# Performance work log

Measured on AMD Instinct MI355X. Metric: run time of the kernel, lower is better.

The kernel has to match this reference:

```python
import jax, jax.numpy as jnp
import numpy as np

CL = 64      # per-object feature dim
N = 8        # num objects/slots
B = 8192     # batch


def _init(key, fan_in, shape):
    # torch Linear default: U(-1/sqrt(fan_in), 1/sqrt(fan_in))
    bound = 1.0 / np.sqrt(fan_in)
    return jax.random.uniform(key, shape, jnp.float32, -bound, bound)


def setup_inputs() -> dict:
    key = jax.random.key(0)
    ks = jax.random.split(key, 20)
    inp = {
        "s": jax.random.normal(ks[0], (B, N, CL), jnp.float32),
        # weights stored (in, out); y = x @ W + b
        "W_enc": _init(ks[1], CL, (CL, CL)),   "b_enc": _init(ks[2], CL, (CL,)),
        "W_self0": _init(ks[3], CL, (CL, CL)), "b_self0": _init(ks[4], CL, (CL,)),
        "W_self1": _init(ks[5], CL, (CL, CL)), "b_self1": _init(ks[6], CL, (CL,)),
        "W_rel0": _init(ks[7], 2 * CL + 1, (2 * CL + 1, 2 * CL)), "b_rel0": _init(ks[8], 2 * CL + 1, (2 * CL,)),
        "W_rel1": _init(ks[9], 2 * CL, (2 * CL, CL)),             "b_rel1": _init(ks[10], 2 * CL, (CL,)),
        "W_rel2": _init(ks[11], CL, (CL, CL)),                    "b_rel2": _init(ks[12], CL, (CL,)),
        "W_att0": _init(ks[13], 2 * CL + 1, (2 * CL + 1, 2 * CL)), "b_att0": _init(ks[14], 2 * CL + 1, (2 * CL,)),
        "W_att1": _init(ks[15], 2 * CL, (2 * CL, CL)),             "b_att1": _init(ks[16], 2 * CL, (CL,)),
        "W_att2": _init(ks[17], CL, (CL, 1)),                      "b_att2": _init(ks[18], CL, (1,)),
    }
    return inp


def reference(s, W_enc, b_enc, W_self0, b_self0, W_self1, b_self1,
              W_rel0, b_rel0, W_rel1, b_rel1, W_rel2, b_rel2,
              W_att0, b_att0, W_att1, b_att1, W_att2, b_att2):
    elu = jax.nn.elu
    # keep first 2 coords (positions), re-encode the rest
    s = jnp.concatenate([s[..., :2], (s @ W_enc + b_enc)[..., 2:]], axis=-1)  # [B,N,CL]

    # self dynamics
    h = elu(s @ W_self0 + b_self0)
    self_dyn = h @ W_self1 + b_self1 + h                                      # [B,N,CL]

    # pairwise squared distances on first two coords: [B,N,N,1]
    pos = s[..., :2]
    dist = jnp.sum((pos[:, :, None, :] - pos[:, None, :, :]) ** 2, axis=-1, keepdims=True)

    # combinations = cat(arg1_i, arg2_j, dist). Split the first linear's weight rows
    # so we never materialize the [B,N,N,2CL+1] concat tensor.
    def pair_linear(W, b):
        Wa, Wb, Wd = W[:CL], W[CL:2 * CL], W[2 * CL]
        return (s @ Wa)[:, :, None, :] + (s @ Wb)[:, None, :, :] + dist * Wd + b

    rel_h1 = elu(pair_linear(W_rel0, b_rel0))        # [B,N,N,2CL]
    rel_h2 = elu(rel_h1 @ W_rel1 + b_rel1)           # [B,N,N,CL]
    rel_f = rel_h2 @ W_rel2 + b_rel2 + rel_h2        # [B,N,N,CL]

    att = elu(pair_linear(W_att0, b_att0))
    att = elu(att @ W_att1 + b_att1)
    att = jax.nn.sigmoid(att @ W_att2 + b_att2)      # [B,N,N,1]

    diag_mask = (1.0 - jnp.eye(N, dtype=s.dtype))[None, :, :, None]
    rel_dyn = jnp.sum(rel_f * diag_mask * att, axis=2)   # [B,N,CL]

    return jnp.sum(self_dyn + rel_dyn, axis=1)           # [B,CL]
```

## Files before the change

### kernel.cpp

```cpp
#include <hip/hip_runtime.h>
#include <math.h>

constexpr int NCL = 64;
constexpr int NN  = 8;
constexpr int NG  = 4;
constexpr int NT  = 1024;

typedef __attribute__((ext_vector_type(4))) float f32x4;
typedef __attribute__((ext_vector_type(8))) short s16x8;
#define MFMA __builtin_amdgcn_mfma_f32_16x16x32_bf16

constexpr int OFF_ENC = 0;
constexpr int OFF_S0  = 1024;
constexpr int OFF_S1  = 2048;
constexpr int OFF_R0  = 3072;
constexpr int OFF_A0  = 7168;
constexpr int OFF_A1  = 11264;
constexpr int OFF_R1  = 13312;
constexpr int OFF_R2  = 15360;

__device__ __forceinline__ float elu_f(float x) { return x > 0.f ? x : __expf(x) - 1.f; }

__device__ __forceinline__ unsigned f2u(float x) { union { float f; unsigned u; } c; c.f = x; return c.u; }
__device__ __forceinline__ float u2f(unsigned u) { union { unsigned u; float f; } c; c.u = u; return c.f; }

__device__ __forceinline__ void splitpack8(const float v[8], s16x8& hi, s16x8& lo) {
    union { s16x8 s; unsigned u[4]; } H, L;
    #pragma unroll
    for (int e = 0; e < 8; e += 2) {
        H.u[e >> 1] = __builtin_amdgcn_perm(f2u(v[e + 1]), f2u(v[e]), 0x07060302u);
        const float t0 = u2f(f2u(v[e])     & 0xffff0000u);
        const float t1 = u2f(f2u(v[e + 1]) & 0xffff0000u);
        L.u[e >> 1] = __builtin_amdgcn_perm(f2u(v[e + 1] - t1), f2u(v[e] - t0), 0x07060302u);
    }
    hi = H.s; lo = L.s;
}

__device__ __forceinline__ void afrag_split(const float* act, int row, int kbase,
                                            s16x8& hi, s16x8& lo) {
    const float4 v0 = *(const float4*)(act + row * 68 + kbase);
    const float4 v1 = *(const float4*)(act + row * 68 + kbase + 4);
    const float v[8] = {v0.x, v0.y, v0.z, v0.w, v1.x, v1.y, v1.z, v1.w};
    splitpack8(v, hi, lo);
}

__device__ __forceinline__ f32x4 node_tile_pk(const float* act, const s16x8* __restrict__ wb,
                                              int mt, int nt, int lane) {
    const int row = mt * 16 + (lane & 15);
    const int g   = lane >> 4;
    f32x4 acc = {0.f, 0.f, 0.f, 0.f};
    #pragma unroll
    for (int kg = 0; kg < 2; ++kg) {
        s16x8 ah, al;
        afrag_split(act, row, kg * 32 + g * 8, ah, al);
        const s16x8 bh = wb[(kg * 4 + nt) * 64 + lane];
        const s16x8 bl = wb[512 + (kg * 4 + nt) * 64 + lane];
        acc = MFMA(ah, bh, acc, 0, 0, 0);
        acc = MFMA(ah, bl, acc, 0, 0, 0);
        acc = MFMA(al, bh, acc, 0, 0, 0);
    }
    return acc;
}

__device__ __forceinline__ void x1frag(const float* Arow, const float* Brow,
                                       const float* wdg, float d, int fbase,
                                       s16x8& hi, s16x8& lo) {
    const float4 a0 = *(const float4*)(Arow + fbase);
    const float4 a1 = *(const float4*)(Arow + fbase + 4);
    const float4 c0 = *(const float4*)(Brow + fbase);
    const float4 c1 = *(const float4*)(Brow + fbase + 4);
    const float4 w0 = *(const float4*)(wdg + fbase);
    const float4 w1 = *(const float4*)(wdg + fbase + 4);
    float v[8];
    v[0] = elu_f(fmaf(d, w0.x, a0.x + c0.x));
    v[1] = elu_f(fmaf(d, w0.y, a0.y + c0.y));
    v[2] = elu_f(fmaf(d, w0.z, a0.z + c0.z));
    v[3] = elu_f(fmaf(d, w0.w, a0.w + c0.w));
    v[4] = elu_f(fmaf(d, w1.x, a1.x + c1.x));
    v[5] = elu_f(fmaf(d, w1.y, a1.y + c1.y));
    v[6] = elu_f(fmaf(d, w1.z, a1.z + c1.z));
    v[7] = elu_f(fmaf(d, w1.w, a1.w + c1.w));
    splitpack8(v, hi, lo);
}

__device__ __forceinline__ short bfh_rn(float x) {
    union { float f; unsigned u; } c; c.f = x;
    return (short)((c.u + 0x7fffu + ((c.u >> 16) & 1u)) >> 16);
}
__device__ __forceinline__ void split_tr(float x, short& hi, short& lo) {
    union { float f; unsigned u; } c; c.f = x;
    hi = (short)(c.u >> 16);
    union { unsigned u; float f; } t; t.u = c.u & 0xffff0000u;
    lo = bfh_rn(x - t.f);
}

__global__ __launch_bounds__(64)
void prep_kernel(const float* __restrict__ We,  const float* __restrict__ Ws0,
                 const float* __restrict__ Ws1, const float* __restrict__ Wr0,
                 const float* __restrict__ Wa0, const float* __restrict__ Wa1,
                 const float* __restrict__ Wr1, const float* __restrict__ Wr2,
                 s16x8* __restrict__ ws)
{
    const int b = blockIdx.x, lane = threadIdx.x;
    const float* W; int nnt, nfrag, base, frag;
    if      (b < 8)   { W = We;  nnt = 4; nfrag = 8;  base = OFF_ENC; frag = b; }
    else if (b < 16)  { W = Ws0; nnt = 4; nfrag = 8;  base = OFF_S0;  frag = b - 8; }
    else if (b < 24)  { W = Ws1; nnt = 4; nfrag = 8;  base = OFF_S1;  frag = b - 16; }
    else if (b < 56)  { W = Wr0; nnt = 8; nfrag = 32; base = OFF_R0;  frag = b - 24; }
    else if (b < 88)  { W = Wa0; nnt = 8; nfrag = 32; base = OFF_A0;  frag = b - 56; }
    else if (b < 104) { W = Wa1; nnt = 4; nfrag = 16; base = OFF_A1;  frag = b - 88; }
    else if (b < 120) { W = Wr1; nnt = 4; nfrag = 16; base = OFF_R1;  frag = b - 104; }
    else              { W = Wr2; nnt = 4; nfrag = 8;  base = OFF_R2;  frag = b - 120; }
    const int kg = frag / nnt, nt = frag % nnt;
    const int N  = nnt * 16;
    const int g  = lane >> 4, col = nt * 16 + (lane & 15);
    s16x8 hi, lo;
    #pragma unroll
    for (int e = 0; e < 8; ++e) {
        short a, c; split_tr(W[(kg * 32 + g * 8 + e) * N + col], a, c);
        hi[e] = a; lo[e] = c;
    }
    ws[base + frag * 64 + lane]              = hi;
    ws[base + nfrag * 64 + frag * 64 + lane] = lo;
}

__global__ __launch_bounds__(NT, 1)
void gh_kernel(const float* __restrict__ S,
               const float* __restrict__ b_enc,
               const float* __restrict__ b_self0, const float* __restrict__ b_self1,
               const float* __restrict__ W_rel0,  const float* __restrict__ b_rel0,
               const float* __restrict__ b_rel1,  const float* __restrict__ b_rel2,
               const float* __restrict__ W_att0,  const float* __restrict__ b_att0,
               const float* __restrict__ b_att1,
               const float* __restrict__ W_att2,  const float* __restrict__ b_att2,
               const s16x8* __restrict__ wp,
               float* __restrict__ Out)
{
    __shared__ __align__(16) float sbuf[32 * 68];
    __shared__ __align__(16) float encb[32 * 68];
    __shared__ __align__(16) float hbuf[32 * 68];
    __shared__ __align__(16) float ABm[4][32 * 132];
    __shared__ __align__(16) s16x8 wstpA[2048];
    __shared__ __align__(16) s16x8 wstpR[2048];
    __shared__ float d2l[4 * 64];
    __shared__ float cntl[32];
    __shared__ float wdl[2][128];

    const int tid  = threadIdx.x;
    const int w    = tid >> 6;
    const int lane = tid & 63;
    const int g    = lane >> 4;
    const int b0   = blockIdx.x * NG;
    float* sd   = sbuf;
    float* Tb   = hbuf;
    float* Ubuf = encb;
    float* Rbuf = encb + 512;

    {
        const float* src = S + (size_t)b0 * NN * NCL;
        for (int idx = tid; idx < 32 * 64; idx += NT)
            sbuf[(idx >> 6) * 68 + (idx & 63)] = src[idx];
        for (int idx = tid; idx < 2048; idx += NT) {
            wstpA[idx] = wp[OFF_A1 + idx];
            wstpR[idx] = wp[OFF_R1 + idx];
        }
        if (tid < 128) {
            wdl[0][tid] = W_rel0[128 * 128 + tid];
            wdl[1][tid] = W_att0[128 * 128 + tid];
        }
    }
    __syncthreads();

    if (tid < 256) {
        const int bi = tid >> 6, i = (tid >> 3) & 7, j = tid & 7;
        const float dx = sbuf[(bi * 8 + i) * 68 + 0] - sbuf[(bi * 8 + j) * 68 + 0];
        const float dy = sbuf[(bi * 8 + i) * 68 + 1] - sbuf[(bi * 8 + j) * 68 + 1];
        d2l[bi * 64 + i * 8 + j] = dx * dx + dy * dy;
    }

    if (w < 8) {
        const int mt = w & 1, nt = w >> 1;
        f32x4 acc = node_tile_pk(sbuf, wp + OFF_ENC, mt, nt, lane);
        const int   col = nt * 16 + (lane & 15);
        const float be  = b_enc[col];
        #pragma unroll
        for (int reg = 0; reg < 4; ++reg) {
            const int row = mt * 16 + g * 4 + reg;
            float v = acc[reg] + be;
            if (col < 2) v = sbuf[row * 68 + col];
            encb[row * 68 + col] = v;
        }
    }
    __syncthreads();

    if (w < 8) {
        const int mt = w & 1, nt = w >> 1;
        f32x4 acc = node_tile_pk(encb, wp + OFF_S0, mt, nt, lane);
        const int   col = nt * 16 + (lane & 15);
        const float bs  = b_self0[col];
        #pragma unroll
        for (int reg = 0; reg < 4; ++reg)
            hbuf[(mt * 16 + g * 4 + reg) * 68 + col] = elu_f(acc[reg] + bs);
    }
    __syncthreads();

    if (w < 8) {
        const int mt = w & 1, nt = w >> 1;
        f32x4 acc = node_tile_pk(hbuf, wp + OFF_S1, mt, nt, lane);
        const int   col = nt * 16 + (lane & 15);
        const float bs  = b_self1[col];
        #pragma unroll
        for (int reg = 0; reg < 4; ++reg) {
            const int row = mt * 16 + g * 4 + reg;
            sd[row * 68 + col] = acc[reg] + bs + hbuf[row * 68 + col];
        }
    }
    {
        const int mtp = w >> 3, ntp = w & 7;
        const int row = mtp * 16 + (lane & 15);
        const int col = ntp * 16 + (lane & 15);
        s16x8 eh[2], el[2];
        afrag_split(encb, row, g * 8, eh[0], el[0]);
        afrag_split(encb, row, 32 + g * 8, eh[1], el[1]);
        #pragma unroll
        for (int m = 0; m < 4; ++m) {
            const s16x8* wb = wp + ((m < 2) ? OFF_R0 : OFF_A0);
            const int kgo = (m & 1) * 2;
            f32x4 acc = {0.f, 0.f, 0.f, 0.f};
            #pragma unroll
            for (int kg = 0; kg < 2; ++kg) {
                const s16x8 bh = wb[((kgo + kg) * 8 + ntp) * 64 + lane];
                const s16x8 bl = wb[2048 + ((kgo + kg) * 8 + ntp) * 64 + lane];
                acc = MFMA(eh[kg], bh, acc, 0, 0, 0);
                acc = MFMA(eh[kg], bl, acc, 0, 0, 0);
                acc = MFMA(el[kg], bh, acc, 0, 0, 0);
            }
            const float badd = (m == 0) ? b_rel0[col] : (m == 2) ? b_att0[col] : 0.f;
            #pragma unroll
            for (int reg = 0; reg < 4; ++reg)
                ABm[m][(mtp * 16 + g * 4 + reg) * 132 + col] = acc[reg] + badd;
        }
    }
    __syncthreads();

    const int bi    = w >> 2;
    const int ihalf = (w >> 1) & 1;
    const int mt    = w & 1;
    const int pp    = (lane & 15) + 16 * mt;
    const int il    = pp >> 3, jj8 = pp & 7;
    const float* Arow_a = &ABm[2][(bi * 8 + ihalf * 4 + il) * 132];
    const float* Brow_a = &ABm[3][(bi * 8 + jj8) * 132];
    const float* Arow_r = &ABm[0][(bi * 8 + ihalf * 4 + il) * 132];
    const float* Brow_r = &ABm[1][(bi * 8 + jj8) * 132];
    const float dpair   = d2l[bi * 64 + (ihalf * 4 + il) * 8 + jj8];

    float attreg[4];
    {
        const float ba2 = b_att2[0];
        float wa2v[4];
        f32x4 acc[4];
        #pragma unroll
        for (int nt = 0; nt < 4; ++nt) {
            wa2v[nt] = W_att2[nt * 16 + (lane & 15)];
            const float b1 = b_att1[nt * 16 + (lane & 15)];
            acc[nt] = {b1, b1, b1, b1};
        }
        #pragma unroll
        for (int kg = 0; kg < 4; ++kg) {
            s16x8 ah, al;
            x1frag(Arow_a, Brow_a, &wdl[1][0], dpair, kg * 32 + g * 8, ah, al);
            #pragma unroll
            for (int nt = 0; nt < 4; ++nt) {
                const s16x8 bh = wstpA[(kg * 4 + nt) * 64 + lane];
                const s16x8 bl = wstpA[1024 + (kg * 4 + nt) * 64 + lane];
                acc[nt] = MFMA(ah, bh, acc[nt], 0, 0, 0);
                acc[nt] = MFMA(ah, bl, acc[nt], 0, 0, 0);
                acc[nt] = MFMA(al, bh, acc[nt], 0, 0, 0);
            }
        }
        #pragma unroll
        for (int reg = 0; reg < 4; ++reg) {
            float s = 0.f;
            #pragma unroll
            for (int nt = 0; nt < 4; ++nt) s += elu_f(acc[nt][reg]) * wa2v[nt];
            s += __shfl_xor(s, 1, 64);
            s += __shfl_xor(s, 2, 64);
            s += __shfl_xor(s, 4, 64);
            s += __shfl_xor(s, 8, 64);
            attreg[reg] = 1.f / (1.f + __expf(-(s + ba2)));
        }
    }
    {
        f32x4 acc[4];
        #pragma unroll
        for (int nt = 0; nt < 4; ++nt) {
            const float b1 = b_rel1[nt * 16 + (lane & 15)];
            acc[nt] = {b1, b1, b1, b1};
        }
        #pragma unroll
        for (int kg = 0; kg < 4; ++kg) {
            s16x8 ah, al;
            x1frag(Arow_r, Brow_r, &wdl[0][0], dpair, kg * 32 + g * 8, ah, al);
            #pragma unroll
            for (int nt = 0; nt < 4; ++nt) {
                const s16x8 bh = wstpR[(kg * 4 + nt) * 64 + lane];
                const s16x8 bl = wstpR[1024 + (kg * 4 + nt) * 64 + lane];
                acc[nt] = MFMA(ah, bh, acc[nt], 0, 0, 0);
                acc[nt] = MFMA(ah, bl, acc[nt], 0, 0, 0);
                acc[nt] = MFMA(al, bh, acc[nt], 0, 0, 0);
            }
        }
        const int ifull = ihalf * 4 + 2 * mt + (g >> 1);
        float coef[4], cpart = 0.f;
        #pragma unroll
        for (int reg = 0; reg < 4; ++reg) {
            const int jj = 4 * (g & 1) + reg;
            coef[reg] = (jj == ifull) ? 0.f : attreg[reg];
            cpart += coef[reg];
        }
        const float csum = cpart + __shfl_xor(cpart, 16, 64);
        if (((g & 1) == 0) && ((lane & 15) == 0))
            cntl[bi * 8 + ifull] = csum;
        #pragma unroll
        for (int nt = 0; nt < 4; ++nt) {
            float tpart = 0.f;
            #pragma unroll
            for (int reg = 0; reg < 4; ++reg)
                tpart += coef[reg] * elu_f(acc[nt][reg]);
            const float tsum = tpart + __shfl_xor(tpart, 16, 64);
            if ((g & 1) == 0)
                Tb[(bi * 8 + ifull) * 68 + nt * 16 + (lane & 15)] = tsum;
        }
    }
    __syncthreads();

    if (tid < 256) {
        const int b = tid >> 6, c = tid & 63;
        float u = 0.f;
        #pragma unroll
        for (int i = 0; i < 8; ++i) u += Tb[(b * 8 + i) * 68 + c];
        Ubuf[b * 68 + c] = u;
    }
    __syncthreads();

    if (w < 4) {
        const int nt2 = w;
        f32x4 acc = {0.f, 0.f, 0.f, 0.f};
        const int row = lane & 15;
        #pragma unroll
        for (int kg = 0; kg < 2; ++kg) {
            float4 q0 = {0.f, 0.f, 0.f, 0.f}, q1 = {0.f, 0.f, 0.f, 0.f};
            if (row < 4) {
                q0 = *(const float4*)(Ubuf + row * 68 + kg * 32 + g * 8);
                q1 = *(const float4*)(Ubuf + row * 68 + kg * 32 + g * 8 + 4);
            }
            const float v[8] = {q0.x, q0.y, q0.z, q0.w, q1.x, q1.y, q1.z, q1.w};
            s16x8 uh, ul;
            splitpack8(v, uh, ul);
            const s16x8 bh = wp[OFF_R2 + (kg * 4 + nt2) * 64 + lane];
            const s16x8 bl = wp[OFF_R2 + 512 + (kg * 4 + nt2) * 64 + lane];
            acc = MFMA(uh, bh, acc, 0, 0, 0);
            acc = MFMA(uh, bl, acc, 0, 0, 0);
            acc = MFMA(ul, bh, acc, 0, 0, 0);
        }
        if (g == 0) {
            #pragma unroll
            for (int reg = 0; reg < 4; ++reg)
                Rbuf[reg * 64 + nt2 * 16 + (lane & 15)] = acc[reg];
        }
    }
    __syncthreads();

    if (tid < 256) {
        const int b = tid >> 6, c = tid & 63;
        float sds = 0.f, C = 0.f;
        #pragma unroll
        for (int i = 0; i < 8; ++i) {
            sds += sd[(b * 8 + i) * 68 + c];
            C   += cntl[b * 8 + i];
        }
        Out[(size_t)(b0 + b) * 64 + c] = sds + Rbuf[b * 64 + c] + C * b_rel2[c] + Ubuf[b * 68 + c];
    }
}

extern "C" void kernel_launch(void* const* d_in, const int* in_sizes, int n_in,
                              void* d_out, int out_size, void* d_ws, size_t ws_size,
                              hipStream_t stream) {
    const float* S       = (const float*)d_in[0];
    const float* W_enc   = (const float*)d_in[1];
    const float* b_enc   = (const float*)d_in[2];
    const float* W_self0 = (const float*)d_in[3];
    const float* b_self0 = (const float*)d_in[4];
    const float* W_self1 = (const float*)d_in[5];
    const float* b_self1 = (const float*)d_in[6];
    const float* W_rel0  = (const float*)d_in[7];
    const float* b_rel0  = (const float*)d_in[8];
    const float* W_rel1  = (const float*)d_in[9];
    const float* b_rel1  = (const float*)d_in[10];
    const float* W_rel2  = (const float*)d_in[11];
    const float* b_rel2  = (const float*)d_in[12];
    const float* W_att0  = (const float*)d_in[13];
    const float* b_att0  = (const float*)d_in[14];
    const float* W_att1  = (const float*)d_in[15];
    const float* b_att1  = (const float*)d_in[16];
    const float* W_att2  = (const float*)d_in[17];
    const float* b_att2  = (const float*)d_in[18];

    s16x8* wpk = (s16x8*)d_ws;

    prep_kernel<<<dim3(128), dim3(64), 0, stream>>>(
        W_enc, W_self0, W_self1, W_rel0, W_att0, W_att1, W_rel1, W_rel2, wpk);

    const int nB   = in_sizes[0] / (NN * NCL);
    const int grid = nB / NG;

    gh_kernel<<<dim3(grid), dim3(NT), 0, stream>>>(
        S, b_enc, b_self0, b_self1,
        W_rel0, b_rel0, b_rel1, b_rel2,
        W_att0, b_att0, b_att1, W_att2, b_att2,
        wpk, (float*)d_out);
}
```

Measured before the change: 223.6 us.

## Halve block size to two batches per block and read pair weights from global

Shrinks each block from 4 batch elements with 1024 threads to 2 batch elements with 512 threads. It also drops the LDS staging of the att1/rel1 weight fragments, which now come straight from global memory (through L1/L2). Together these cut LDS use per block so several blocks can share a CU, with launch bounds raised to allow that. The cost is repeated global loads of the weight fragments in the inner MFMA loop and some per-block setup overhead repeated across twice as many blocks.

```diff
diff --git a/kernel.cpp b/kernel.cpp
--- a/kernel.cpp
+++ b/kernel.cpp
@@ -3,8 +3,8 @@
 
 constexpr int NCL = 64;
 constexpr int NN  = 8;
-constexpr int NG  = 4;
-constexpr int NT  = 1024;
+constexpr int NG  = 2;
+constexpr int NT  = 512;
 
 typedef __attribute__((ext_vector_type(4))) float f32x4;
 typedef __attribute__((ext_vector_type(8))) short s16x8;
@@ -124,7 +124,7 @@
     ws[base + nfrag * 64 + frag * 64 + lane] = lo;
 }
 
-__global__ __launch_bounds__(NT, 1)
+__global__ __launch_bounds__(NT, 6)
 void gh_kernel(const float* __restrict__ S,
                const float* __restrict__ b_enc,
                const float* __restrict__ b_self0, const float* __restrict__ b_self1,
@@ -136,14 +136,12 @@
                const s16x8* __restrict__ wp,
                float* __restrict__ Out)
 {
-    __shared__ __align__(16) float sbuf[32 * 68];
-    __shared__ __align__(16) float encb[32 * 68];
-    __shared__ __align__(16) float hbuf[32 * 68];
-    __shared__ __align__(16) float ABm[4][32 * 132];
-    __shared__ __align__(16) s16x8 wstpA[2048];
-    __shared__ __align__(16) s16x8 wstpR[2048];
-    __shared__ float d2l[4 * 64];
-    __shared__ float cntl[32];
+    __shared__ __align__(16) float sbuf[16 * 68];
+    __shared__ __align__(16) float encb[16 * 68];
+    __shared__ __align__(16) float hbuf[16 * 68];
+    __shared__ __align__(16) float ABm[4][16 * 132];
+    __shared__ float d2l[2 * 64];
+    __shared__ float cntl[16];
     __shared__ float wdl[2][128];
 
     const int tid  = threadIdx.x;
@@ -158,12 +156,8 @@
 
     {
         const float* src = S + (size_t)b0 * NN * NCL;
-        for (int idx = tid; idx < 32 * 64; idx += NT)
+        for (int idx = tid; idx < 16 * 64; idx += NT)
             sbuf[(idx >> 6) * 68 + (idx & 63)] = src[idx];
-        for (int idx = tid; idx < 2048; idx += NT) {
-            wstpA[idx] = wp[OFF_A1 + idx];
-            wstpR[idx] = wp[OFF_R1 + idx];
-        }
         if (tid < 128) {
             wdl[0][tid] = W_rel0[128 * 128 + tid];
             wdl[1][tid] = W_att0[128 * 128 + tid];
@@ -171,21 +165,21 @@
     }
     __syncthreads();
 
-    if (tid < 256) {
+    if (tid < 128) {
         const int bi = tid >> 6, i = (tid >> 3) & 7, j = tid & 7;
         const float dx = sbuf[(bi * 8 + i) * 68 + 0] - sbuf[(bi * 8 + j) * 68 + 0];
         const float dy = sbuf[(bi * 8 + i) * 68 + 1] - sbuf[(bi * 8 + j) * 68 + 1];
         d2l[bi * 64 + i * 8 + j] = dx * dx + dy * dy;
     }
 
-    if (w < 8) {
-        const int mt = w & 1, nt = w >> 1;
-        f32x4 acc = node_tile_pk(sbuf, wp + OFF_ENC, mt, nt, lane);
+    if (w < 4) {
+        const int nt = w;
+        f32x4 acc = node_tile_pk(sbuf, wp + OFF_ENC, 0, nt, lane);
         const int   col = nt * 16 + (lane & 15);
         const float be  = b_enc[col];
         #pragma unroll
         for (int reg = 0; reg < 4; ++reg) {
-            const int row = mt * 16 + g * 4 + reg;
+            const int row = g * 4 + reg;
             float v = acc[reg] + be;
             if (col < 2) v = sbuf[row * 68 + col];
             encb[row * 68 + col] = v;
@@ -193,31 +187,31 @@
     }
     __syncthreads();
 
-    if (w < 8) {
-        const int mt = w & 1, nt = w >> 1;
-        f32x4 acc = node_tile_pk(encb, wp + OFF_S0, mt, nt, lane);
+    if (w < 4) {
+        const int nt = w;
+        f32x4 acc = node_tile_pk(encb, wp + OFF_S0, 0, nt, lane);
         const int   col = nt * 16 + (lane & 15);
         const float bs  = b_self0[col];
         #pragma unroll
         for (int reg = 0; reg < 4; ++reg)
-            hbuf[(mt * 16 + g * 4 + reg) * 68 + col] = elu_f(acc[reg] + bs);
-    }
-    __syncthreads();
-
-    if (w < 8) {
-        const int mt = w & 1, nt = w >> 1;
-        f32x4 acc = node_tile_pk(hbuf, wp + OFF_S1, mt, nt, lane);
+            hbuf[(g * 4 + reg) * 68 + col] = elu_f(acc[reg] + bs);
+    }
+    __syncthreads();
+
+    if (w < 4) {
+        const int nt = w;
+        f32x4 acc = node_tile_pk(hbuf, wp + OFF_S1, 0, nt, lane);
         const int   col = nt * 16 + (lane & 15);
         const float bs  = b_self1[col];
         #pragma unroll
         for (int reg = 0; reg < 4; ++reg) {
-            const int row = mt * 16 + g * 4 + reg;
+            const int row = g * 4 + reg;
             sd[row * 68 + col] = acc[reg] + bs + hbuf[row * 68 + col];
         }
     }
     {
-        const int mtp = w >> 3, ntp = w & 7;
-        const int row = mtp * 16 + (lane & 15);
+        const int ntp = w;
+        const int row = lane & 15;
         const int col = ntp * 16 + (lane & 15);
         s16x8 eh[2], el[2];
         afrag_split(encb, row, g * 8, eh[0], el[0]);
@@ -238,7 +232,7 @@
             const float badd = (m == 0) ? b_rel0[col] : (m == 2) ? b_att0[col] : 0.f;
             #pragma unroll
             for (int reg = 0; reg < 4; ++reg)
-                ABm[m][(mtp * 16 + g * 4 + reg) * 132 + col] = acc[reg] + badd;
+                ABm[m][(g * 4 + reg) * 132 + col] = acc[reg] + badd;
         }
     }
     __syncthreads();
@@ -271,8 +265,8 @@
             x1frag(Arow_a, Brow_a, &wdl[1][0], dpair, kg * 32 + g * 8, ah, al);
             #pragma unroll
             for (int nt = 0; nt < 4; ++nt) {
-                const s16x8 bh = wstpA[(kg * 4 + nt) * 64 + lane];
-                const s16x8 bl = wstpA[1024 + (kg * 4 + nt) * 64 + lane];
+                const s16x8 bh = wp[OFF_A1 + (kg * 4 + nt) * 64 + lane];
+                const s16x8 bl = wp[OFF_A1 + 1024 + (kg * 4 + nt) * 64 + lane];
                 acc[nt] = MFMA(ah, bh, acc[nt], 0, 0, 0);
                 acc[nt] = MFMA(ah, bl, acc[nt], 0, 0, 0);
                 acc[nt] = MFMA(al, bh, acc[nt], 0, 0, 0);
@@ -303,8 +297,8 @@
             x1frag(Arow_r, Brow_r, &wdl[0][0], dpair, kg * 32 + g * 8, ah, al);
             #pragma unroll
             for (int nt = 0; nt < 4; ++nt) {
-                const s16x8 bh = wstpR[(kg * 4 + nt) * 64 + lane];
-                const s16x8 bl = wstpR[1024 + (kg * 4 + nt) * 64 + lane];
+                const s16x8 bh = wp[OFF_R1 + (kg * 4 + nt) * 64 + lane];
+                const s16x8 bl = wp[OFF_R1 + 1024 + (kg * 4 + nt) * 64 + lane];
                 acc[nt] = MFMA(ah, bh, acc[nt], 0, 0, 0);
                 acc[nt] = MFMA(ah, bl, acc[nt], 0, 0, 0);
                 acc[nt] = MFMA(al, bh, acc[nt], 0, 0, 0);
@@ -334,7 +328,7 @@
     }
     __syncthreads();
 
-    if (tid < 256) {
+    if (tid < 128) {
         const int b = tid >> 6, c = tid & 63;
         float u = 0.f;
         #pragma unroll
@@ -350,7 +344,7 @@
         #pragma unroll
         for (int kg = 0; kg < 2; ++kg) {
             float4 q0 = {0.f, 0.f, 0.f, 0.f}, q1 = {0.f, 0.f, 0.f, 0.f};
-            if (row < 4) {
+            if (row < 2) {
                 q0 = *(const float4*)(Ubuf + row * 68 + kg * 32 + g * 8);
                 q1 = *(const float4*)(Ubuf + row * 68 + kg * 32 + g * 8 + 4);
             }
@@ -365,13 +359,13 @@
         }
         if (g == 0) {
             #pragma unroll
-            for (int reg = 0; reg < 4; ++reg)
+            for (int reg = 0; reg < 2; ++reg)
                 Rbuf[reg * 64 + nt2 * 16 + (lane & 15)] = acc[reg];
         }
     }
     __syncthreads();
 
-    if (tid < 256) {
+    if (tid < 128) {
         const int b = tid >> 6, c = tid & 63;
         float sds = 0.f, C = 0.f;
         #pragma unroll
```

Measured after the change: 209.0 us. 1.07x faster.
